# Kernel optimization log

Hardware: AMD Instinct MI355X
Metric: run time of the kernel (lower is better)

Reference implementation:

```python
import jax, jax.numpy as jnp
import numpy as np

B_BASE = 512   # queries
F_IN = 16      # incoming beam width
F_OUT = 16     # outgoing beam width (cfg.B)
D = 128        # vector dim
DH = 256       # MLP hidden dim
KCB = 4096     # codebook size
A = 32         # n_codes: approximate top-k shortlist
M = 2          # previous code steps
L = 2          # residual blocks


def setup_inputs() -> dict:
    key = jax.random.key(0)
    ks = jax.random.split(key, 16)
    s = 0.05
    return {
        "x_BD": jax.random.normal(ks[0], (B_BASE, D), jnp.float32),
        "xhat_BFD": jax.random.normal(ks[1], (B_BASE, F_IN, D), jnp.float32),
        "codes_MBF": jax.random.randint(ks[2], (M, B_BASE, F_IN), 0, KCB),
        "codebook": jax.random.normal(ks[3], (KCB, D), jnp.float32) * s,
        "codebook_rq": jax.random.normal(ks[4], (KCB, D), jnp.float32) * s,
        "in_w": jax.random.normal(ks[5], (D, DH), jnp.float32) * s,
        "in_b": jnp.zeros((DH,), jnp.float32),
        "cc_w": jax.random.normal(ks[6], (DH + D, DH), jnp.float32) * s,
        "cc_b": jnp.zeros((DH,), jnp.float32),
        "rb_w1": jax.random.normal(ks[7], (L, DH, DH), jnp.float32) * s,
        "rb_b1": jnp.zeros((L, DH), jnp.float32),
        "rb_w2": jax.random.normal(ks[8], (L, DH, DH), jnp.float32) * s,
        "rb_b2": jnp.zeros((L, DH), jnp.float32),
        "out_w": jax.random.normal(ks[9], (DH, D), jnp.float32) * s,
        "out_b": jnp.zeros((D,), jnp.float32),
    }


def reference(x_BD, xhat_BFD, codes_MBF, codebook, codebook_rq,
              in_w, in_b, cc_w, cc_b, rb_w1, rb_b1, rb_w2, rb_b2,
              out_w, out_b):
    B_base, F, Dd = xhat_BFD.shape
    B = B_base * F
    xhat_BD = xhat_BFD.reshape(B, Dd)

    # --- stage 1: approximate pairwise distance (drops ||x||^2 term) + shortlist topk ---
    xt_BD = (x_BD[:, None, :] - xhat_BFD).reshape(B, Dd)           # residual targets
    cb_sq = jnp.sum(codebook_rq * codebook_rq, axis=-1)             # [K]
    dists_BK = cb_sq[None, :] - 2.0 * (xt_BD @ codebook_rq.T)       # [B, K]
    _, top_codes_BA = jax.lax.top_k(-dists_BK, A)                   # smallest-A -> [B, A]

    # --- stage 2: gather codewords, run small residual MLP on candidates ---
    cw_in = codebook[top_codes_BA].reshape(B_base, F, A, Dd)        # [Bb,F,A,D]
    h = cw_in @ in_w + in_b                                         # in_proj -> [Bb,F,A,DH]
    xb = jnp.broadcast_to(xhat_BFD[:, :, None, :], (B_base, F, A, Dd))
    h = jnp.concatenate([h, xb], axis=-1) @ cc_w + cc_b             # concat block
    for i in range(rb_w1.shape[0]):
        h = h + jax.nn.relu(h @ rb_w1[i] + rb_b1[i]) @ rb_w2[i] + rb_b2[i]
    cw = h @ out_w + out_b + cw_in                                   # out_proj + residual codeword

    # --- stage 3: exact-ish distance over beam*A candidates + beam topk ---
    cw = cw.reshape(B, A, Dd) + xhat_BD[:, None, :]                  # candidate reconstructions
    cw_flat = cw.reshape(B_base, F * A, Dd)
    d2 = jnp.sum(cw_flat * cw_flat, axis=-1) - 2.0 * jnp.einsum('bd,bkd->bk', x_BD, cw_flat)
    _, idx_BF = jax.lax.top_k(-d2, F_OUT)                            # [Bb, F_OUT]

    # --- stage 4: regather codes and reconstructions for surviving beams ---
    codes_g_BF = jnp.take_along_axis(top_codes_BA.reshape(B_base, F * A), idx_BF, axis=-1)
    codes_rep = jnp.repeat(codes_MBF, A, axis=-1)                    # [M,Bb,F*A]
    idx_M = jnp.broadcast_to(idx_BF[None], (codes_MBF.shape[0], B_base, F_OUT))
    codes_sel = jnp.take_along_axis(codes_rep, idx_M, axis=-1)       # [M,Bb,F_OUT]
    xhat_next = jnp.take_along_axis(cw_flat, idx_BF[:, :, None], axis=1)  # [Bb,F_OUT,D]
    codes_out = jnp.concatenate([codes_sel, codes_g_BF[None]], axis=0)    # [M+1,Bb,F_OUT]
    return xhat_next, codes_out
```

## Files before the change

kernel.cpp:

```cpp
#include <hip/hip_runtime.h>
#include <float.h>

typedef unsigned int u32;
typedef unsigned long long u64;
typedef unsigned short u16;
typedef __attribute__((ext_vector_type(8))) short s16x8;
typedef __attribute__((ext_vector_type(4))) float f32x4;


static __device__ __forceinline__ u32 ordu(float f) {
  u32 u = __float_as_uint(f);
  return u ^ (u32)(((int)u >> 31) | (int)0x80000000);
}
static __device__ __forceinline__ u16 f2bf(float f) {
  u32 b = __float_as_uint(f);
  b += 0x7fffu + ((b >> 16) & 1u);
  return (u16)(b >> 16);
}


__global__ __launch_bounds__(256) void k_cbrqT(const float* __restrict__ cbrq,
                                               float* __restrict__ cbT) {
  __shared__ float tile[128 * 33];
  const int k0 = blockIdx.x * 32;
  const int t = threadIdx.x;
#pragma unroll
  for (int rep = 0; rep < 16; ++rep) {
    const int flat = rep * 256 + t;
    const int kk = flat >> 7, d = flat & 127;
    tile[d * 33 + kk] = cbrq[(k0 + kk) * 128 + d];
  }
  __syncthreads();
#pragma unroll
  for (int rep = 0; rep < 16; ++rep) {
    const int flat = rep * 256 + t;
    const int d = flat >> 5, kk = flat & 31;
    cbT[d * 4096 + k0 + kk] = tile[d * 33 + kk];
  }
}

__global__ __launch_bounds__(256) void k_cbsq(const float* __restrict__ cbT,
                                              float* __restrict__ cb_sq) {
  const int k = blockIdx.x * 256 + threadIdx.x;
  float r[8];
#pragma unroll
  for (int j = 0; j < 8; ++j) {
    const float v = cbT[j * 4096 + k];
    r[j] = __fmul_rn(v, v);
  }
  for (int i = 8; i < 128; i += 8) {
#pragma unroll
    for (int j = 0; j < 8; ++j) {
      const float v = cbT[(i + j) * 4096 + k];
      r[j] = __fadd_rn(r[j], __fmul_rn(v, v));
    }
  }
  cb_sq[k] = __fadd_rn(
      __fadd_rn(__fadd_rn(r[0], r[1]), __fadd_rn(r[2], r[3])),
      __fadd_rn(__fadd_rn(r[4], r[5]), __fadd_rn(r[6], r[7])));
}

__global__ __launch_bounds__(256) void k_xt(const float* __restrict__ x,
                                            const float* __restrict__ xhat,
                                            float* __restrict__ xt) {
  const int i = blockIdx.x * 256 + threadIdx.x;
  const int row = i >> 5, d4 = i & 31;
  const float4 a = ((const float4*)x)[(row >> 4) * 32 + d4];
  const float4 b = ((const float4*)xhat)[i];
  float4 r;
  r.x = __fsub_rn(a.x, b.x); r.y = __fsub_rn(a.y, b.y);
  r.z = __fsub_rn(a.z, b.z); r.w = __fsub_rn(a.w, b.w);
  ((float4*)xt)[i] = r;
}

__global__ __launch_bounds__(256) void k_codeh(const float* __restrict__ cb,
                                               const float* __restrict__ in_w,
                                               const float* __restrict__ in_b,
                                               float* __restrict__ tmp_h) {
  __shared__ float row[128];
  const int code = blockIdx.x;
  const int t = threadIdx.x;
  if (t < 128) row[t] = cb[code * 128 + t];
  __syncthreads();
  float a = 0.f;
  for (int d = 0; d < 128; ++d) a = __builtin_fmaf(row[d], in_w[d * 256 + t], a);
  tmp_h[code * 256 + t] = __fadd_rn(a, in_b[t]);
}

__global__ __launch_bounds__(256) void k_pack(const float* __restrict__ rb_w1,
                                              const float* __restrict__ out_w,
                                              float* __restrict__ Wcat) {
  const int i = blockIdx.x;
  const int t = threadIdx.x;
  Wcat[i * 640 + t] = rb_w1[i * 256 + t];
  Wcat[i * 640 + 256 + t] = rb_w1[65536 + i * 256 + t];
  if (t < 128) Wcat[i * 640 + 512 + t] = out_w[i * 128 + t];
}

__global__ __launch_bounds__(256) void k_biasprep(
    const float* __restrict__ rb_b1, const float* __restrict__ rb_b2,
    const float* __restrict__ rb_w1, const float* __restrict__ out_w,
    const float* __restrict__ out_b, const float* __restrict__ cc_b,
    const float* __restrict__ Wcat, float* __restrict__ cvec) {
  const int t = threadIdx.x;
  const float* w11 = rb_w1 + 65536;
  float b2v = rb_b1[256 + t];
  for (int i = 0; i < 256; ++i) b2v += rb_b2[i] * w11[i * 256 + t];
  float c0 = rb_b1[t], c1 = b2v;
  for (int i = 0; i < 256; ++i) {
    const float cbi = cc_b[i];
    c0 += cbi * Wcat[i * 640 + t];
    c1 += cbi * Wcat[i * 640 + 256 + t];
  }
  cvec[t] = c0;
  cvec[256 + t] = c1;
  if (t < 128) {
    float bDv = out_b[t];
    for (int i = 0; i < 256; ++i)
      bDv += (rb_b2[i] + rb_b2[256 + i]) * out_w[i * 128 + t];
    float c2 = bDv;
    for (int i = 0; i < 256; ++i) c2 += cc_b[i] * Wcat[i * 640 + 512 + t];
    cvec[512 + t] = c2;
  }
}

__global__ __launch_bounds__(256) void k_wfrag(
    const float* __restrict__ W21, const float* __restrict__ V1,
    const float* __restrict__ V2, u16* __restrict__ W21f,
    u16* __restrict__ V1f, u16* __restrict__ V2f) {
  const int gid = blockIdx.x * 256 + threadIdx.x;
  const int l = gid & 63;
  const int grp = gid >> 6;
  const int kq = (l >> 4) * 8;
  const int nn = l & 15;
  if (grp < 128) {
    const int kt = grp >> 4, nt = grp & 15;
    u16* dst = W21f + (size_t)(grp * 64 + l) * 8;
#pragma unroll
    for (int j = 0; j < 8; ++j)
      dst[j] = f2bf(W21[(kt * 32 + kq + j) * 256 + nt * 16 + nn]);
  } else if (grp < 192) {
    const int g2 = grp - 128, kt = g2 >> 3, nt = g2 & 7;
    u16* dst = V1f + (size_t)(g2 * 64 + l) * 8;
#pragma unroll
    for (int j = 0; j < 8; ++j)
      dst[j] = f2bf(V1[(kt * 32 + kq + j) * 128 + nt * 16 + nn]);
  } else {
    const int g2 = grp - 192, kt = g2 >> 3, nt = g2 & 7;
    u16* dst = V2f + (size_t)(g2 * 64 + l) * 8;
#pragma unroll
    for (int j = 0; j < 8; ++j)
      dst[j] = f2bf(V2[(kt * 32 + kq + j) * 128 + nt * 16 + nn]);
  }
}

__global__ __launch_bounds__(256, 4) void gemm_f32(
    const float* __restrict__ Am, const float* __restrict__ Bm,
    float* __restrict__ Cm, const int Mi, const int Ni, const int Ki,
    const float* __restrict__ bias, const float* __restrict__ addm) {
  __shared__ float As[16][68];
  __shared__ float Bs[16][68];
  const int m0 = blockIdx.x * 64, n0 = blockIdx.y * 64;
  const int t = threadIdx.x;
  const int tm = (t & 15) * 4, tn = (t >> 4) * 4;
  float acc[4][4] = {};
  for (int k0 = 0; k0 < Ki; k0 += 16) {
    {
      const int row = t >> 2, q = t & 3;
      const float4 a4 = *(const float4*)(Am + (size_t)(m0 + row) * Ki + k0 + q * 4);
      As[q * 4 + 0][row] = a4.x; As[q * 4 + 1][row] = a4.y;
      As[q * 4 + 2][row] = a4.z; As[q * 4 + 3][row] = a4.w;
      const int kk = t >> 4, n4 = t & 15;
      *(float4*)&Bs[kk][n4 * 4] =
          *(const float4*)(Bm + (size_t)(k0 + kk) * Ni + n0 + n4 * 4);
    }
    __syncthreads();
#pragma unroll
    for (int kk = 0; kk < 16; ++kk) {
      const float4 av = *(const float4*)&As[kk][tm];
      const float4 bv = *(const float4*)&Bs[kk][tn];
      const float aa[4] = {av.x, av.y, av.z, av.w};
      const float bb[4] = {bv.x, bv.y, bv.z, bv.w};
#pragma unroll
      for (int i = 0; i < 4; ++i)
#pragma unroll
        for (int j = 0; j < 4; ++j) acc[i][j] += aa[i] * bb[j];
    }
    __syncthreads();
  }
#pragma unroll
  for (int i = 0; i < 4; ++i) {
    const int m = m0 + tm + i;
#pragma unroll
    for (int j = 0; j < 4; ++j) {
      const int n = n0 + tn + j;
      float v = acc[i][j];
      if (bias) v += bias[n];
      if (addm) v += addm[(size_t)m * Ni + n];
      Cm[(size_t)m * Ni + n] = v;
    }
  }
}

__global__ __launch_bounds__(256, 4) void gemm_scatter(
    const float* __restrict__ Am, const float* __restrict__ Bm, const int Mi,
    const int Ki, const float* __restrict__ bias,
    const float* __restrict__ add3, float* __restrict__ O1,
    float* __restrict__ O2, float* __restrict__ O3) {
  __shared__ float As[16][68];
  __shared__ float Bs[16][68];
  const int m0 = blockIdx.x * 64, n0 = blockIdx.y * 64;
  const int t = threadIdx.x;
  const int tm = (t & 15) * 4, tn = (t >> 4) * 4;
  float acc[4][4] = {};
  for (int k0 = 0; k0 < Ki; k0 += 16) {
    {
      const int row = t >> 2, q = t & 3;
      const float4 a4 = *(const float4*)(Am + (size_t)(m0 + row) * Ki + k0 + q * 4);
      As[q * 4 + 0][row] = a4.x; As[q * 4 + 1][row] = a4.y;
      As[q * 4 + 2][row] = a4.z; As[q * 4 + 3][row] = a4.w;
      const int kk = t >> 4, n4 = t & 15;
      *(float4*)&Bs[kk][n4 * 4] =
          *(const float4*)(Bm + (size_t)(k0 + kk) * 640 + n0 + n4 * 4);
    }
    __syncthreads();
#pragma unroll
    for (int kk = 0; kk < 16; ++kk) {
      const float4 av = *(const float4*)&As[kk][tm];
      const float4 bv = *(const float4*)&Bs[kk][tn];
      const float aa[4] = {av.x, av.y, av.z, av.w};
      const float bb[4] = {bv.x, bv.y, bv.z, bv.w};
#pragma unroll
      for (int i = 0; i < 4; ++i)
#pragma unroll
        for (int j = 0; j < 4; ++j) acc[i][j] += aa[i] * bb[j];
    }
    __syncthreads();
  }
#pragma unroll
  for (int i = 0; i < 4; ++i) {
    const int m = m0 + tm + i;
#pragma unroll
    for (int j = 0; j < 4; ++j) {
      const int n = n0 + tn + j;
      float v = acc[i][j];
      if (bias) v += bias[n];
      if (n < 256) {
        O1[(size_t)m * 256 + n] = v;
      } else if (n < 512) {
        O2[(size_t)m * 256 + n - 256] = v;
      } else {
        if (add3) v += add3[(size_t)m * 128 + n - 512];
        O3[(size_t)m * 128 + n - 512] = v;
      }
    }
  }
}

__global__ __launch_bounds__(512, 2) void k_stage1(
    const float* __restrict__ xt, const float* __restrict__ cbT,
    const float* __restrict__ cb_sq, int* __restrict__ topc) {
  __shared__ u32 distL[4 * 4096];
  __shared__ float xtL[512];
  const int r0 = blockIdx.x * 4;
  const int t = threadIdx.x;
  xtL[t] = xt[r0 * 128 + t];
  __syncthreads();
  {
    const int k0 = t * 8;
    float acc[4][8] = {};
    for (int d = 0; d < 128; ++d) {
      const float4 c0 = *(const float4*)&cbT[d * 4096 + k0];
      const float4 c1 = *(const float4*)&cbT[d * 4096 + k0 + 4];
      const float cv[8] = {c0.x, c0.y, c0.z, c0.w, c1.x, c1.y, c1.z, c1.w};
      const float x0 = xtL[d], x1 = xtL[128 + d], x2 = xtL[256 + d],
                  x3 = xtL[384 + d];
#pragma unroll
      for (int j = 0; j < 8; ++j) {
        acc[0][j] = __builtin_fmaf(x0, cv[j], acc[0][j]);
        acc[1][j] = __builtin_fmaf(x1, cv[j], acc[1][j]);
        acc[2][j] = __builtin_fmaf(x2, cv[j], acc[2][j]);
        acc[3][j] = __builtin_fmaf(x3, cv[j], acc[3][j]);
      }
    }
    const float4 s0 = *(const float4*)&cb_sq[k0];
    const float4 s1 = *(const float4*)&cb_sq[k0 + 4];
    const float cs[8] = {s0.x, s0.y, s0.z, s0.w, s1.x, s1.y, s1.z, s1.w};
#pragma unroll
    for (int rr = 0; rr < 4; ++rr)
#pragma unroll
      for (int j = 0; j < 8; ++j)
        distL[rr * 4096 + k0 + j] =
            ordu(__fsub_rn(cs[j], __fmul_rn(2.0f, acc[rr][j])));
  }
  __syncthreads();
  const int w = t >> 6, lane = t & 63;
  if (w < 4) {
    u32* dr = distL + w * 4096;
    u64 m1 = ~0ull, m2 = ~0ull;
    for (int e = 0; e < 64; ++e) {
      const int idx = e * 64 + lane;
      const u64 key = ((u64)dr[idx] << 32) | (u32)idx;
      if (key < m1) { m2 = m1; m1 = key; } else if (key < m2) { m2 = key; }
    }
    bool have2 = true;
    for (int it = 0; it < 32; ++it) {
      u64 g = m1;
#pragma unroll
      for (int sh = 1; sh < 64; sh <<= 1) {
        const u64 o = __shfl_xor(g, sh);
        g = (o < g) ? o : g;
      }
      const int bi = (int)(g & 0xFFFFFFFFu);
      if (lane == 0) topc[(r0 + w) * 32 + it] = bi;
      if ((bi & 63) == lane) {
        dr[bi] = 0xFFFFFFFFu;
        if (have2) {
          m1 = m2; m2 = ~0ull; have2 = false;
        } else {
          m1 = m2 = ~0ull;
          for (int e = 0; e < 64; ++e) {
            const int idx = e * 64 + lane;
            const u64 key = ((u64)dr[idx] << 32) | (u32)idx;
            if (key < m1) { m2 = m1; m1 = key; } else if (key < m2) { m2 = key; }
          }
          have2 = true;
        }
      }
    }
  }
}

__global__ __launch_bounds__(256, 4) void k_mlp(
    const int* __restrict__ topc, const float* __restrict__ A1,
    const float* __restrict__ A2, const float* __restrict__ B1,
    const float* __restrict__ B2, const float* __restrict__ Dc,
    const float* __restrict__ Dr, const u16* __restrict__ W21f,
    const u16* __restrict__ V1f, const u16* __restrict__ V2f,
    const float* __restrict__ xhat, const float* __restrict__ x,
    float* __restrict__ d2g) {
  __shared__ __align__(16) u16 abuf[32 * 264];
  __shared__ float B1r[256];
  __shared__ int codesL[32];
  __shared__ float d2red[32][4];

  const int tt = threadIdx.x;
  const int br = blockIdx.x;
  const int bb = br >> 4;
  const int w = tt >> 6, l = tt & 63;

  B1r[tt] = B1[br * 256 + tt];
  if (tt < 32) codesL[tt] = topc[br * 32 + tt];
  __syncthreads();

  {
    const int c = tt & 31, g = tt >> 5;
    const int code = codesL[c];
    const float4* A14 = (const float4*)(A1 + code * 256 + g * 32);
    u32* dst = (u32*)(abuf + c * 264 + g * 32);
#pragma unroll
    for (int e4 = 0; e4 < 8; ++e4) {
      const float4 a = A14[e4];
      const int i = g * 32 + e4 * 4;
      const u32 p0 = (u32)f2bf(fmaxf(a.x + B1r[i], 0.f)) |
                     ((u32)f2bf(fmaxf(a.y + B1r[i + 1], 0.f)) << 16);
      const u32 p1 = (u32)f2bf(fmaxf(a.z + B1r[i + 2], 0.f)) |
                     ((u32)f2bf(fmaxf(a.w + B1r[i + 3], 0.f)) << 16);
      dst[e4 * 2] = p0;
      dst[e4 * 2 + 1] = p1;
    }
  }
  __syncthreads();

  const int arow = l & 15;
  const int kq = (l >> 4) * 8;
  const s16x8* wf = (const s16x8*)W21f;
  const s16x8* v1f = (const s16x8*)V1f;
  const s16x8* v2f = (const s16x8*)V2f;
  const f32x4 zero4 = {0.f, 0.f, 0.f, 0.f};

  f32x4 accf[2][4];
#pragma unroll
  for (int mt = 0; mt < 2; ++mt)
#pragma unroll
    for (int ntl = 0; ntl < 4; ++ntl) accf[mt][ntl] = zero4;
  for (int kt = 0; kt < 8; ++kt) {
    const s16x8 a0 = *(const s16x8*)(abuf + arow * 264 + kt * 32 + kq);
    const s16x8 a1 = *(const s16x8*)(abuf + (16 + arow) * 264 + kt * 32 + kq);
#pragma unroll
    for (int ntl = 0; ntl < 4; ++ntl) {
      const s16x8 b = wf[(kt * 16 + w * 4 + ntl) * 64 + l];
      accf[0][ntl] =
          __builtin_amdgcn_mfma_f32_16x16x32_bf16(a0, b, accf[0][ntl], 0, 0, 0);
      accf[1][ntl] =
          __builtin_amdgcn_mfma_f32_16x16x32_bf16(a1, b, accf[1][ntl], 0, 0, 0);
    }
  }

  f32x4 acc2f[2][2];
#pragma unroll
  for (int mt = 0; mt < 2; ++mt)
#pragma unroll
    for (int ntl = 0; ntl < 2; ++ntl) acc2f[mt][ntl] = zero4;
  for (int kt = 0; kt < 8; ++kt) {
    const s16x8 a0 = *(const s16x8*)(abuf + arow * 264 + kt * 32 + kq);
    const s16x8 a1 = *(const s16x8*)(abuf + (16 + arow) * 264 + kt * 32 + kq);
#pragma unroll
    for (int ntl = 0; ntl < 2; ++ntl) {
      const s16x8 b = v1f[(kt * 8 + w * 2 + ntl) * 64 + l];
      acc2f[0][ntl] = __builtin_amdgcn_mfma_f32_16x16x32_bf16(
          a0, b, acc2f[0][ntl], 0, 0, 0);
      acc2f[1][ntl] = __builtin_amdgcn_mfma_f32_16x16x32_bf16(
          a1, b, acc2f[1][ntl], 0, 0, 0);
    }
  }

  u16 r2v[2][4][4];
#pragma unroll
  for (int mt = 0; mt < 2; ++mt)
#pragma unroll
    for (int ntl = 0; ntl < 4; ++ntl) {
      const int n = w * 64 + ntl * 16 + arow;
      const float b2 = B2[br * 256 + n];
      const f32x4 cf = accf[mt][ntl];
#pragma unroll
      for (int rg = 0; rg < 4; ++rg) {
        const int m = mt * 16 + (l >> 4) * 4 + rg;
        const float a2 = A2[codesL[m] * 256 + n];
        r2v[mt][ntl][rg] = f2bf(fmaxf(cf[rg] + a2 + b2, 0.f));
      }
    }
  __syncthreads();
#pragma unroll
  for (int mt = 0; mt < 2; ++mt)
#pragma unroll
    for (int ntl = 0; ntl < 4; ++ntl) {
      const int n = w * 64 + ntl * 16 + arow;
#pragma unroll
      for (int rg = 0; rg < 4; ++rg) {
        const int m = mt * 16 + (l >> 4) * 4 + rg;
        abuf[m * 264 + n] = r2v[mt][ntl][rg];
      }
    }
  __syncthreads();

  for (int kt = 0; kt < 8; ++kt) {
    const s16x8 a0 = *(const s16x8*)(abuf + arow * 264 + kt * 32 + kq);
    const s16x8 a1 = *(const s16x8*)(abuf + (16 + arow) * 264 + kt * 32 + kq);
#pragma unroll
    for (int ntl = 0; ntl < 2; ++ntl) {
      const s16x8 b = v2f[(kt * 8 + w * 2 + ntl) * 64 + l];
      acc2f[0][ntl] = __builtin_amdgcn_mfma_f32_16x16x32_bf16(
          a0, b, acc2f[0][ntl], 0, 0, 0);
      acc2f[1][ntl] = __builtin_amdgcn_mfma_f32_16x16x32_bf16(
          a1, b, acc2f[1][ntl], 0, 0, 0);
    }
  }

  float sm[2][4];
#pragma unroll
  for (int mt = 0; mt < 2; ++mt)
#pragma unroll
    for (int rg = 0; rg < 4; ++rg) sm[mt][rg] = 0.f;
#pragma unroll
  for (int ntl = 0; ntl < 2; ++ntl) {
    const int d = w * 32 + ntl * 16 + arow;
    const float dr = Dr[br * 128 + d];
    const float xh = xhat[br * 128 + d];
    const float xq = x[bb * 128 + d];
#pragma unroll
    for (int mt = 0; mt < 2; ++mt) {
      const f32x4 cf = acc2f[mt][ntl];
#pragma unroll
      for (int rg = 0; rg < 4; ++rg) {
        const int m = mt * 16 + (l >> 4) * 4 + rg;
        const float cand = cf[rg] + Dc[codesL[m] * 128 + d] + dr + xh;
        sm[mt][rg] += cand * cand - 2.f * xq * cand;
      }
    }
  }
#pragma unroll
  for (int mt = 0; mt < 2; ++mt)
#pragma unroll
    for (int rg = 0; rg < 4; ++rg) {
      float s = sm[mt][rg];
      s += __shfl_xor(s, 1);
      s += __shfl_xor(s, 2);
      s += __shfl_xor(s, 4);
      s += __shfl_xor(s, 8);
      if (arow == 0) d2red[mt * 16 + (l >> 4) * 4 + rg][w] = s;
    }
  __syncthreads();
  if (tt < 32)
    d2g[bb * 512 + (br & 15) * 32 + tt] =
        d2red[tt][0] + d2red[tt][1] + d2red[tt][2] + d2red[tt][3];
}

__global__ __launch_bounds__(64, 1) void k_sel32(const float* __restrict__ d2g,
                                                 int* __restrict__ sel32) {
  __shared__ u32 d2u[512];
  const int bb = blockIdx.x;
  const int t = threadIdx.x;
  for (int i = t; i < 512; i += 64) d2u[i] = ordu(d2g[bb * 512 + i]);
  __syncthreads();
  for (int it = 0; it < 32; ++it) {
    u64 m = ~0ull;
#pragma unroll
    for (int e = 0; e < 8; ++e) {
      const int idx = e * 64 + t;
      const u64 key = ((u64)d2u[idx] << 32) | (u32)idx;
      m = (key < m) ? key : m;
    }
#pragma unroll
    for (int sh = 1; sh < 64; sh <<= 1) {
      const u64 o = __shfl_xor(m, sh);
      m = (o < m) ? o : m;
    }
    const int s = (int)(m & 0xFFFFFFFFu);
    if ((s & 63) == t) d2u[s] = 0xFFFFFFFFu;
    if (t == 0) sel32[bb * 32 + it] = s;
  }
}

__global__ __launch_bounds__(256, 5) void k_rescore(
    const int* __restrict__ sel32, const int* __restrict__ topc,
    const float* __restrict__ tmp_h, const float* __restrict__ cb,
    const float* __restrict__ xhat, const float* __restrict__ x,
    const float* __restrict__ cc_w, const float* __restrict__ cc_b,
    const float* __restrict__ rb_w1, const float* __restrict__ rb_b1,
    const float* __restrict__ rb_w2, const float* __restrict__ rb_b2,
    const float* __restrict__ out_w, const float* __restrict__ out_b,
    float* __restrict__ d2r, float* __restrict__ candv) {
  __shared__ float A_[8][256], B_[8][256], C_[8][256];
  __shared__ float xhL[8][128], xqL[128];
  __shared__ int codeL[8], rowL[8];
  const int bb = blockIdx.x >> 2;
  const int j0 = (blockIdx.x & 3) * 8;
  const int t = threadIdx.x;
  if (t < 8) {
    const int s = sel32[bb * 32 + j0 + t];
    rowL[t] = bb * 16 + (s >> 5);
    codeL[t] = topc[(bb * 16 + (s >> 5)) * 32 + (s & 31)];
  }
  if (t < 128) xqL[t] = x[bb * 128 + t];
  __syncthreads();
  for (int idx = t; idx < 1024; idx += 256) {
    const int c = idx >> 7, d = idx & 127;
    xhL[c][d] = xhat[rowL[c] * 128 + d];
  }
  for (int idx = t; idx < 2048; idx += 256) {
    const int c = idx >> 8, i = idx & 255;
    A_[c][i] = tmp_h[codeL[c] * 256 + i];
  }
  __syncthreads();
  {
    float acc[8] = {};
    for (int i = 0; i < 256; i += 4) {
      const float w0 = cc_w[(i + 0) * 256 + t], w1 = cc_w[(i + 1) * 256 + t];
      const float w2 = cc_w[(i + 2) * 256 + t], w3 = cc_w[(i + 3) * 256 + t];
#pragma unroll
      for (int c = 0; c < 8; ++c) {
        const float4 h = *(const float4*)&A_[c][i];
        acc[c] = __builtin_fmaf(h.x, w0, acc[c]);
        acc[c] = __builtin_fmaf(h.y, w1, acc[c]);
        acc[c] = __builtin_fmaf(h.z, w2, acc[c]);
        acc[c] = __builtin_fmaf(h.w, w3, acc[c]);
      }
    }
    for (int d = 0; d < 128; d += 4) {
      const float w0 = cc_w[(256 + d + 0) * 256 + t];
      const float w1 = cc_w[(256 + d + 1) * 256 + t];
      const float w2 = cc_w[(256 + d + 2) * 256 + t];
      const float w3 = cc_w[(256 + d + 3) * 256 + t];
#pragma unroll
      for (int c = 0; c < 8; ++c) {
        const float4 h = *(const float4*)&xhL[c][d];
        acc[c] = __builtin_fmaf(h.x, w0, acc[c]);
        acc[c] = __builtin_fmaf(h.y, w1, acc[c]);
        acc[c] = __builtin_fmaf(h.z, w2, acc[c]);
        acc[c] = __builtin_fmaf(h.w, w3, acc[c]);
      }
    }
    const float b = cc_b[t];
#pragma unroll
    for (int c = 0; c < 8; ++c) B_[c][t] = __fadd_rn(acc[c], b);
  }
  __syncthreads();
  {
    float acc[8] = {};
    for (int i = 0; i < 256; i += 4) {
      const float w0 = rb_w1[(i + 0) * 256 + t], w1 = rb_w1[(i + 1) * 256 + t];
      const float w2 = rb_w1[(i + 2) * 256 + t], w3 = rb_w1[(i + 3) * 256 + t];
#pragma unroll
      for (int c = 0; c < 8; ++c) {
        const float4 h = *(const float4*)&B_[c][i];
        acc[c] = __builtin_fmaf(h.x, w0, acc[c]);
        acc[c] = __builtin_fmaf(h.y, w1, acc[c]);
        acc[c] = __builtin_fmaf(h.z, w2, acc[c]);
        acc[c] = __builtin_fmaf(h.w, w3, acc[c]);
      }
    }
    const float b = rb_b1[t];
#pragma unroll
    for (int c = 0; c < 8; ++c) C_[c][t] = fmaxf(__fadd_rn(acc[c], b), 0.f);
  }
  __syncthreads();
  {
    float acc[8] = {};
    for (int i = 0; i < 256; i += 4) {
      const float w0 = rb_w2[(i + 0) * 256 + t], w1 = rb_w2[(i + 1) * 256 + t];
      const float w2 = rb_w2[(i + 2) * 256 + t], w3 = rb_w2[(i + 3) * 256 + t];
#pragma unroll
      for (int c = 0; c < 8; ++c) {
        const float4 h = *(const float4*)&C_[c][i];
        acc[c] = __builtin_fmaf(h.x, w0, acc[c]);
        acc[c] = __builtin_fmaf(h.y, w1, acc[c]);
        acc[c] = __builtin_fmaf(h.z, w2, acc[c]);
        acc[c] = __builtin_fmaf(h.w, w3, acc[c]);
      }
    }
    const float b = rb_b2[t];
#pragma unroll
    for (int c = 0; c < 8; ++c)
      A_[c][t] = __fadd_rn(__fadd_rn(B_[c][t], acc[c]), b);
  }
  __syncthreads();
  {
    float acc[8] = {};
    const float* w11 = rb_w1 + 65536;
    for (int i = 0; i < 256; i += 4) {
      const float w0 = w11[(i + 0) * 256 + t], w1 = w11[(i + 1) * 256 + t];
      const float w2 = w11[(i + 2) * 256 + t], w3 = w11[(i + 3) * 256 + t];
#pragma unroll
      for (int c = 0; c < 8; ++c) {
        const float4 h = *(const float4*)&A_[c][i];
        acc[c] = __builtin_fmaf(h.x, w0, acc[c]);
        acc[c] = __builtin_fmaf(h.y, w1, acc[c]);
        acc[c] = __builtin_fmaf(h.z, w2, acc[c]);
        acc[c] = __builtin_fmaf(h.w, w3, acc[c]);
      }
    }
    const float b = rb_b1[256 + t];
#pragma unroll
    for (int c = 0; c < 8; ++c) B_[c][t] = fmaxf(__fadd_rn(acc[c], b), 0.f);
  }
  __syncthreads();
  {
    float acc[8] = {};
    const float* w21 = rb_w2 + 65536;
    for (int i = 0; i < 256; i += 4) {
      const float w0 = w21[(i + 0) * 256 + t], w1 = w21[(i + 1) * 256 + t];
      const float w2 = w21[(i + 2) * 256 + t], w3 = w21[(i + 3) * 256 + t];
#pragma unroll
      for (int c = 0; c < 8; ++c) {
        const float4 h = *(const float4*)&B_[c][i];
        acc[c] = __builtin_fmaf(h.x, w0, acc[c]);
        acc[c] = __builtin_fmaf(h.y, w1, acc[c]);
        acc[c] = __builtin_fmaf(h.z, w2, acc[c]);
        acc[c] = __builtin_fmaf(h.w, w3, acc[c]);
      }
    }
    const float b = rb_b2[256 + t];
#pragma unroll
    for (int c = 0; c < 8; ++c)
      C_[c][t] = __fadd_rn(__fadd_rn(A_[c][t], acc[c]), b);
  }
  __syncthreads();
  if (t < 128) {
    float acc[8] = {};
    for (int i = 0; i < 256; i += 4) {
      const float w0 = out_w[(i + 0) * 128 + t], w1 = out_w[(i + 1) * 128 + t];
      const float w2 = out_w[(i + 2) * 128 + t], w3 = out_w[(i + 3) * 128 + t];
#pragma unroll
      for (int c = 0; c < 8; ++c) {
        const float4 h = *(const float4*)&C_[c][i];
        acc[c] = __builtin_fmaf(h.x, w0, acc[c]);
        acc[c] = __builtin_fmaf(h.y, w1, acc[c]);
        acc[c] = __builtin_fmaf(h.z, w2, acc[c]);
        acc[c] = __builtin_fmaf(h.w, w3, acc[c]);
      }
    }
    const float ob = out_b[t];
#pragma unroll
    for (int c = 0; c < 8; ++c) {
      const float cbv = cb[codeL[c] * 128 + t];
      const float cw_ = __fadd_rn(__fadd_rn(acc[c], ob), cbv);
      const float cand = __fadd_rn(cw_, xhL[c][t]);
      B_[c][t] = cand;
      candv[(bb * 32 + j0 + c) * 128 + t] = cand;
    }
  }
  __syncthreads();
  if (t < 8) {
    float r[8];
#pragma unroll
    for (int j = 0; j < 8; ++j) {
      const float v = B_[t][j];
      r[j] = __fmul_rn(v, v);
    }
    for (int i = 8; i < 128; i += 8) {
#pragma unroll
      for (int j = 0; j < 8; ++j) {
        const float v = B_[t][i + j];
        r[j] = __fadd_rn(r[j], __fmul_rn(v, v));
      }
    }
    const float s1f = __fadd_rn(
        __fadd_rn(__fadd_rn(r[0], r[1]), __fadd_rn(r[2], r[3])),
        __fadd_rn(__fadd_rn(r[4], r[5]), __fadd_rn(r[6], r[7])));
    double s2 = 0.0;
    for (int d = 0; d < 128; ++d)
      s2 += (double)xqL[d] * (double)B_[t][d];
    const float s2f = (float)s2;
    d2r[bb * 32 + j0 + t] = __fsub_rn(s1f, __fmul_rn(2.0f, s2f));
  }
}

__global__ __launch_bounds__(64, 1) void k_final(
    const float* __restrict__ d2r, const int* __restrict__ sel32,
    const int* __restrict__ topc, const int* __restrict__ codes_in,
    const float* __restrict__ candv, float* __restrict__ out) {
  __shared__ u32 winLo[16];
  const int bb = blockIdx.x;
  const int t = threadIdx.x;
  u64 key = ~0ull;
  if (t < 32) {
    const u32 s = (u32)sel32[bb * 32 + t];
    key = ((u64)ordu(d2r[bb * 32 + t]) << 32) | (s << 5) | (u32)t;
  }
  for (int it = 0; it < 16; ++it) {
    u64 m = key;
#pragma unroll
    for (int sh = 1; sh < 64; sh <<= 1) {
      const u64 o = __shfl_xor(m, sh);
      m = (o < m) ? o : m;
    }
    if (key == m) key = ~0ull;
    if (t == 0) winLo[it] = (u32)(m & 0xFFFFFFFFu);
  }
  __syncthreads();
  if (t < 16) {
    const u32 lo = winLo[t];
    const int s = (int)((lo >> 5) & 511u);
    const int f = s >> 5;
    const int code = topc[(bb * 16 + f) * 32 + (s & 31)];
    float* oc = out + 512 * 16 * 128;
    oc[bb * 16 + t] = (float)codes_in[bb * 16 + f];
    oc[8192 + bb * 16 + t] = (float)codes_in[8192 + bb * 16 + f];
    oc[16384 + bb * 16 + t] = (float)code;
  }
  __syncthreads();
  for (int idx = t; idx < 2048; idx += 64) {
    const int w_ = idx >> 7, d = idx & 127;
    const int j = (int)(winLo[w_] & 31u);
    out[(bb * 16 + w_) * 128 + d] = candv[(bb * 32 + j) * 128 + d];
  }
}

extern "C" void kernel_launch(void* const* d_in, const int* in_sizes, int n_in,
                              void* d_out, int out_size, void* d_ws,
                              size_t ws_size, hipStream_t stream) {
  const float* x = (const float*)d_in[0];
  const float* xhat = (const float*)d_in[1];
  const int* codes = (const int*)d_in[2];
  const float* cb = (const float*)d_in[3];
  const float* cbrq = (const float*)d_in[4];
  const float* in_w = (const float*)d_in[5];
  const float* in_b = (const float*)d_in[6];
  const float* cc_w = (const float*)d_in[7];
  const float* cc_b = (const float*)d_in[8];
  const float* rb_w1 = (const float*)d_in[9];
  const float* rb_b1 = (const float*)d_in[10];
  const float* rb_w2 = (const float*)d_in[11];
  const float* rb_b2 = (const float*)d_in[12];
  const float* out_w = (const float*)d_in[13];
  const float* out_b = (const float*)d_in[14];
  float* out = (float*)d_out;

  float* ws = (float*)d_ws;
  size_t o = 0;
  float* cb_sq = ws + o; o += 4096;
  float* xt = ws + o;    const size_t xt_off = o; o += (size_t)8192 * 128;
  float* cbT = ws + o;   o += (size_t)128 * 4096;
  float* tmp_h = ws + o; o += (size_t)4096 * 256;
  float* Wcat = ws + o;  o += (size_t)256 * 640;
  float* M_A = ws + o;   o += (size_t)256 * 640;
  float* M_B = ws + o;   o += (size_t)128 * 640;
  float* cvec = ws + o;  o += 640;
  float* A1 = ws + o;    o += (size_t)4096 * 256;
  float* A2 = ws + o;    o += (size_t)4096 * 256;
  float* Dc = ws + o;    o += (size_t)4096 * 128;
  float* B1 = ws + o;    o += (size_t)8192 * 256;
  float* B2 = ws + o;    o += (size_t)8192 * 256;
  float* Dr = ws + o;    o += (size_t)8192 * 128;
  float* W21 = ws + o;   o += 65536;
  float* V1 = ws + o;    o += 32768;
  float* V2 = ws + o;    o += 32768;
  int* topc = (int*)(ws + o); o += 262144;
  float* d2g = ws + o;   o += 262144;
  u16* W21f = (u16*)(ws + o); o += 32768;
  u16* V1f = (u16*)(ws + o);  o += 16384;
  u16* V2f = (u16*)(ws + o);  o += 16384;
  float* candv = ws + o; o += (size_t)16384 * 128;
  float* d2r = ws + xt_off;
  int* sel32 = (int*)(ws + xt_off + 16384);

  k_cbrqT<<<dim3(128), dim3(256), 0, stream>>>(cbrq, cbT);
  k_cbsq<<<dim3(16), dim3(256), 0, stream>>>(cbT, cb_sq);
  k_xt<<<dim3(1024), dim3(256), 0, stream>>>(x, xhat, xt);
  k_codeh<<<dim3(4096), dim3(256), 0, stream>>>(cb, in_w, in_b, tmp_h);
  k_pack<<<dim3(256), dim3(256), 0, stream>>>(rb_w1, out_w, Wcat);
  k_biasprep<<<dim3(1), dim3(256), 0, stream>>>(rb_b1, rb_b2, rb_w1, out_w,
                                                out_b, cc_b, Wcat, cvec);
  gemm_f32<<<dim3(4, 10), dim3(256), 0, stream>>>(cc_w, Wcat, M_A, 256, 640,
                                                  256, nullptr, nullptr);
  gemm_f32<<<dim3(2, 10), dim3(256), 0, stream>>>(cc_w + 256 * 256, Wcat, M_B,
                                                  128, 640, 256, nullptr,
                                                  nullptr);
  gemm_scatter<<<dim3(64, 10), dim3(256), 0, stream>>>(
      tmp_h, M_A, 4096, 256, nullptr, cb, A1, A2, Dc);
  gemm_scatter<<<dim3(128, 10), dim3(256), 0, stream>>>(
      xhat, M_B, 8192, 128, cvec, nullptr, B1, B2, Dr);
  gemm_f32<<<dim3(4, 4), dim3(256), 0, stream>>>(rb_w2, rb_w1 + 65536, W21, 256,
                                                 256, 256, nullptr, nullptr);
  gemm_f32<<<dim3(4, 2), dim3(256), 0, stream>>>(rb_w2, out_w, V1, 256, 128,
                                                 256, nullptr, nullptr);
  gemm_f32<<<dim3(4, 2), dim3(256), 0, stream>>>(rb_w2 + 65536, out_w, V2, 256,
                                                 128, 256, nullptr, nullptr);
  k_wfrag<<<dim3(64), dim3(256), 0, stream>>>(W21, V1, V2, W21f, V1f, V2f);

  k_stage1<<<dim3(2048), dim3(512), 0, stream>>>(xt, cbT, cb_sq, topc);
  k_mlp<<<dim3(8192), dim3(256), 0, stream>>>(topc, A1, A2, B1, B2, Dc, Dr,
                                              W21f, V1f, V2f, xhat, x, d2g);
  k_sel32<<<dim3(512), dim3(64), 0, stream>>>(d2g, sel32);
  k_rescore<<<dim3(2048), dim3(256), 0, stream>>>(
      sel32, topc, tmp_h, cb, xhat, x, cc_w, cc_b, rb_w1, rb_b1, rb_w2, rb_b2,
      out_w, out_b, d2r, candv);
  k_final<<<dim3(512), dim3(64), 0, stream>>>(d2r, sel32, topc, codes, candv,
                                              out);
  (void)in_sizes; (void)n_in; (void)out_size; (void)ws_size;
}
```

Measured before the change: 892.0 us.

## Fuse prep kernels and precompute per-code cc_w projection for rescore

Folds the codebook squared-norm computation into the transpose kernel and computes the residual targets inside k_stage1, which removes two launches and the xt workspace round trip. k_codeh now also computes P = tmp_h @ cc_w[:256] once per codeword. k_rescore then gathers one row of P per candidate instead of redoing a 256x256 matvec for each of the 16384 selected candidates. The cost is extra per-code work and a larger workspace buffer for P.

```diff
diff --git a/kernel.cpp b/kernel.cpp
--- a/kernel.cpp
+++ b/kernel.cpp
@@ -20,7 +20,8 @@
 
 
 __global__ __launch_bounds__(256) void k_cbrqT(const float* __restrict__ cbrq,
-                                               float* __restrict__ cbT) {
+                                               float* __restrict__ cbT,
+                                               float* __restrict__ cb_sq) {
   __shared__ float tile[128 * 33];
   const int k0 = blockIdx.x * 32;
   const int t = threadIdx.x;
@@ -37,54 +38,54 @@
     const int d = flat >> 5, kk = flat & 31;
     cbT[d * 4096 + k0 + kk] = tile[d * 33 + kk];
   }
-}
-
-__global__ __launch_bounds__(256) void k_cbsq(const float* __restrict__ cbT,
-                                              float* __restrict__ cb_sq) {
-  const int k = blockIdx.x * 256 + threadIdx.x;
-  float r[8];
-#pragma unroll
-  for (int j = 0; j < 8; ++j) {
-    const float v = cbT[j * 4096 + k];
-    r[j] = __fmul_rn(v, v);
-  }
-  for (int i = 8; i < 128; i += 8) {
+  if (t < 32) {
+    float r[8];
 #pragma unroll
     for (int j = 0; j < 8; ++j) {
-      const float v = cbT[(i + j) * 4096 + k];
-      r[j] = __fadd_rn(r[j], __fmul_rn(v, v));
-    }
-  }
-  cb_sq[k] = __fadd_rn(
-      __fadd_rn(__fadd_rn(r[0], r[1]), __fadd_rn(r[2], r[3])),
-      __fadd_rn(__fadd_rn(r[4], r[5]), __fadd_rn(r[6], r[7])));
-}
-
-__global__ __launch_bounds__(256) void k_xt(const float* __restrict__ x,
-                                            const float* __restrict__ xhat,
-                                            float* __restrict__ xt) {
-  const int i = blockIdx.x * 256 + threadIdx.x;
-  const int row = i >> 5, d4 = i & 31;
-  const float4 a = ((const float4*)x)[(row >> 4) * 32 + d4];
-  const float4 b = ((const float4*)xhat)[i];
-  float4 r;
-  r.x = __fsub_rn(a.x, b.x); r.y = __fsub_rn(a.y, b.y);
-  r.z = __fsub_rn(a.z, b.z); r.w = __fsub_rn(a.w, b.w);
-  ((float4*)xt)[i] = r;
+      const float v = tile[j * 33 + t];
+      r[j] = __fmul_rn(v, v);
+    }
+    for (int i = 8; i < 128; i += 8) {
+#pragma unroll
+      for (int j = 0; j < 8; ++j) {
+        const float v = tile[(i + j) * 33 + t];
+        r[j] = __fadd_rn(r[j], __fmul_rn(v, v));
+      }
+    }
+    cb_sq[k0 + t] = __fadd_rn(
+        __fadd_rn(__fadd_rn(r[0], r[1]), __fadd_rn(r[2], r[3])),
+        __fadd_rn(__fadd_rn(r[4], r[5]), __fadd_rn(r[6], r[7])));
+  }
 }
 
 __global__ __launch_bounds__(256) void k_codeh(const float* __restrict__ cb,
                                                const float* __restrict__ in_w,
                                                const float* __restrict__ in_b,
-                                               float* __restrict__ tmp_h) {
+                                               const float* __restrict__ cc_w,
+                                               float* __restrict__ tmp_h,
+                                               float* __restrict__ P) {
   __shared__ float row[128];
+  __shared__ float th[256];
   const int code = blockIdx.x;
   const int t = threadIdx.x;
   if (t < 128) row[t] = cb[code * 128 + t];
   __syncthreads();
   float a = 0.f;
   for (int d = 0; d < 128; ++d) a = __builtin_fmaf(row[d], in_w[d * 256 + t], a);
-  tmp_h[code * 256 + t] = __fadd_rn(a, in_b[t]);
+  const float thv = __fadd_rn(a, in_b[t]);
+  tmp_h[code * 256 + t] = thv;
+  th[t] = thv;
+  __syncthreads();
+  float p = 0.f;
+  for (int i = 0; i < 256; i += 4) {
+    const float w0 = cc_w[(i + 0) * 256 + t], w1 = cc_w[(i + 1) * 256 + t];
+    const float w2 = cc_w[(i + 2) * 256 + t], w3 = cc_w[(i + 3) * 256 + t];
+    p = __builtin_fmaf(th[i + 0], w0, p);
+    p = __builtin_fmaf(th[i + 1], w1, p);
+    p = __builtin_fmaf(th[i + 2], w2, p);
+    p = __builtin_fmaf(th[i + 3], w3, p);
+  }
+  P[code * 256 + t] = p;
 }
 
 __global__ __launch_bounds__(256) void k_pack(const float* __restrict__ rb_w1,
@@ -258,13 +259,17 @@
 }
 
 __global__ __launch_bounds__(512, 2) void k_stage1(
-    const float* __restrict__ xt, const float* __restrict__ cbT,
-    const float* __restrict__ cb_sq, int* __restrict__ topc) {
+    const float* __restrict__ x, const float* __restrict__ xhat,
+    const float* __restrict__ cbT, const float* __restrict__ cb_sq,
+    int* __restrict__ topc) {
   __shared__ u32 distL[4 * 4096];
   __shared__ float xtL[512];
   const int r0 = blockIdx.x * 4;
   const int t = threadIdx.x;
-  xtL[t] = xt[r0 * 128 + t];
+  {
+    const int rr = r0 + (t >> 7), d = t & 127;
+    xtL[t] = __fsub_rn(x[(rr >> 4) * 128 + d], xhat[rr * 128 + d]);
+  }
   __syncthreads();
   {
     const int k0 = t * 8;
@@ -524,7 +529,7 @@
 
 __global__ __launch_bounds__(256, 5) void k_rescore(
     const int* __restrict__ sel32, const int* __restrict__ topc,
-    const float* __restrict__ tmp_h, const float* __restrict__ cb,
+    const float* __restrict__ P, const float* __restrict__ cb,
     const float* __restrict__ xhat, const float* __restrict__ x,
     const float* __restrict__ cc_w, const float* __restrict__ cc_b,
     const float* __restrict__ rb_w1, const float* __restrict__ rb_b1,
@@ -548,25 +553,11 @@
     const int c = idx >> 7, d = idx & 127;
     xhL[c][d] = xhat[rowL[c] * 128 + d];
   }
-  for (int idx = t; idx < 2048; idx += 256) {
-    const int c = idx >> 8, i = idx & 255;
-    A_[c][i] = tmp_h[codeL[c] * 256 + i];
-  }
   __syncthreads();
   {
-    float acc[8] = {};
-    for (int i = 0; i < 256; i += 4) {
-      const float w0 = cc_w[(i + 0) * 256 + t], w1 = cc_w[(i + 1) * 256 + t];
-      const float w2 = cc_w[(i + 2) * 256 + t], w3 = cc_w[(i + 3) * 256 + t];
-#pragma unroll
-      for (int c = 0; c < 8; ++c) {
-        const float4 h = *(const float4*)&A_[c][i];
-        acc[c] = __builtin_fmaf(h.x, w0, acc[c]);
-        acc[c] = __builtin_fmaf(h.y, w1, acc[c]);
-        acc[c] = __builtin_fmaf(h.z, w2, acc[c]);
-        acc[c] = __builtin_fmaf(h.w, w3, acc[c]);
-      }
-    }
+    float acc[8];
+#pragma unroll
+    for (int c = 0; c < 8; ++c) acc[c] = P[codeL[c] * 256 + t];
     for (int d = 0; d < 128; d += 4) {
       const float w0 = cc_w[(256 + d + 0) * 256 + t];
       const float w1 = cc_w[(256 + d + 1) * 256 + t];
@@ -780,8 +771,8 @@
   float* ws = (float*)d_ws;
   size_t o = 0;
   float* cb_sq = ws + o; o += 4096;
-  float* xt = ws + o;    const size_t xt_off = o; o += (size_t)8192 * 128;
-  float* cbT = ws + o;   o += (size_t)128 * 4096;
+  float* P = ws + o;     o += (size_t)4096 * 256;
+  float* cbT = ws + o;   const size_t cbT_off = o; o += (size_t)128 * 4096;
   float* tmp_h = ws + o; o += (size_t)4096 * 256;
   float* Wcat = ws + o;  o += (size_t)256 * 640;
   float* M_A = ws + o;   o += (size_t)256 * 640;
@@ -802,13 +793,11 @@
   u16* V1f = (u16*)(ws + o);  o += 16384;
   u16* V2f = (u16*)(ws + o);  o += 16384;
   float* candv = ws + o; o += (size_t)16384 * 128;
-  float* d2r = ws + xt_off;
-  int* sel32 = (int*)(ws + xt_off + 16384);
-
-  k_cbrqT<<<dim3(128), dim3(256), 0, stream>>>(cbrq, cbT);
-  k_cbsq<<<dim3(16), dim3(256), 0, stream>>>(cbT, cb_sq);
-  k_xt<<<dim3(1024), dim3(256), 0, stream>>>(x, xhat, xt);
-  k_codeh<<<dim3(4096), dim3(256), 0, stream>>>(cb, in_w, in_b, tmp_h);
+  float* d2r = ws + cbT_off;
+  int* sel32 = (int*)(ws + cbT_off + 16384);
+
+  k_cbrqT<<<dim3(128), dim3(256), 0, stream>>>(cbrq, cbT, cb_sq);
+  k_codeh<<<dim3(4096), dim3(256), 0, stream>>>(cb, in_w, in_b, cc_w, tmp_h, P);
   k_pack<<<dim3(256), dim3(256), 0, stream>>>(rb_w1, out_w, Wcat);
   k_biasprep<<<dim3(1), dim3(256), 0, stream>>>(rb_b1, rb_b2, rb_w1, out_w,
                                                 out_b, cc_b, Wcat, cvec);
@@ -829,12 +818,12 @@
                                                  128, 256, nullptr, nullptr);
   k_wfrag<<<dim3(64), dim3(256), 0, stream>>>(W21, V1, V2, W21f, V1f, V2f);
 
-  k_stage1<<<dim3(2048), dim3(512), 0, stream>>>(xt, cbT, cb_sq, topc);
+  k_stage1<<<dim3(2048), dim3(512), 0, stream>>>(x, xhat, cbT, cb_sq, topc);
   k_mlp<<<dim3(8192), dim3(256), 0, stream>>>(topc, A1, A2, B1, B2, Dc, Dr,
                                               W21f, V1f, V2f, xhat, x, d2g);
   k_sel32<<<dim3(512), dim3(64), 0, stream>>>(d2g, sel32);
   k_rescore<<<dim3(2048), dim3(256), 0, stream>>>(
-      sel32, topc, tmp_h, cb, xhat, x, cc_w, cc_b, rb_w1, rb_b1, rb_w2, rb_b2,
+      sel32, topc, P, cb, xhat, x, cc_w, cc_b, rb_w1, rb_b1, rb_w2, rb_b2,
       out_w, out_b, d2r, candv);
   k_final<<<dim3(512), dim3(64), 0, stream>>>(d2r, sel32, topc, codes, candv,
                                               out);
```

Result: no change. 878.4 us (-1.5%).
